# Kernel tuning notes

Measured on AMD Instinct MI355X. Metric: run time of the kernel, lower is better.

The kernel has to match this reference:

```python
import jax, jax.numpy as jnp
import numpy as np

B, T, D, H = 8, 4096, 1024, 1024


def setup_inputs() -> dict:
    key = jax.random.key(0)
    ks = jax.random.split(key, 8)
    s = 1.0 / np.sqrt(D)
    x = jax.random.normal(ks[0], (B, T, D), dtype=jnp.float32)
    Wq = jax.random.uniform(ks[1], (H, D), jnp.float32, -s, s)
    bq = jax.random.uniform(ks[2], (H,), jnp.float32, -s, s)
    Wk = jax.random.uniform(ks[3], (H, D), jnp.float32, -s, s)
    bk = jax.random.uniform(ks[4], (H,), jnp.float32, -s, s)
    Wv = jax.random.uniform(ks[5], (H, D), jnp.float32, -s, s)
    bv = jax.random.uniform(ks[6], (H,), jnp.float32, -s, s)
    wbias = jax.random.uniform(ks[7], (H,), jnp.float32, 0.0, 1.0)  # torch.rand
    return {"x": x, "Wq": Wq, "bq": bq, "Wk": Wk, "bk": bk, "Wv": Wv, "bv": bv, "wbias": wbias}


def reference(x, Wq, bq, Wk, bk, Wv, bv, wbias):
    # Q, K, V: [B, T, H]
    Q = jnp.einsum('btd,hd->bth', x, Wq) + bq
    K = jnp.einsum('btd,hd->bth', x, Wk) + bk
    V = jnp.einsum('btd,hd->bth', x, Wv) + bv
    Q_sig = jax.nn.sigmoid(Q)
    numer = jnp.exp(K + wbias)            # [B, T, H]
    denom = numer.sum(axis=0)             # [T, H] (faithful: sum over batch axis)
    weighted = (numer * V).sum(axis=0) / denom  # [T, H]
    Yt = Q_sig * weighted                 # broadcast -> [B, T, H]
    return Yt  # to_out is Identity since dim == hidden_dim
```

## Files before the change

### kernel.cpp

```cpp
#include <hip/hip_runtime.h>
#include <hip/hip_bf16.h>

#define B_ 8
#define T_ 4096
#define D_ 1024
#define H_ 1024

typedef __attribute__((ext_vector_type(8))) short short8;
typedef __attribute__((ext_vector_type(4))) float floatx4;

#define GLOAD16(gptr, lptr) \
  __builtin_amdgcn_global_load_lds((const __attribute__((address_space(1))) void*)(gptr), \
                                   (__attribute__((address_space(3))) void*)(lptr), 16, 0, 0)

__device__ __forceinline__ ushort f2b(float f) {
  unsigned x = __builtin_bit_cast(unsigned, f);
  unsigned r = (x + 0x7fffu + ((x >> 16) & 1u)) >> 16;
  return (ushort)r;
}
__device__ __forceinline__ float b2f(ushort u) {
  return __builtin_bit_cast(float, (unsigned)u << 16);
}

__global__ void cvt_kernel(const float* __restrict__ in, ushort* __restrict__ out, int n) {
  int idx = blockIdx.x * blockDim.x + threadIdx.x;
  int stride = gridDim.x * blockDim.x;
  for (long i = (long)idx * 8; i < n; i += (long)stride * 8) {
    const float4 f0 = *(const float4*)(in + i);
    const float4 f1 = *(const float4*)(in + i + 4);
    union { ushort u[8]; uint4 v; } r;
    r.u[0] = f2b(f0.x); r.u[1] = f2b(f0.y); r.u[2] = f2b(f0.z); r.u[3] = f2b(f0.w);
    r.u[4] = f2b(f1.x); r.u[5] = f2b(f1.y); r.u[6] = f2b(f1.z); r.u[7] = f2b(f1.w);
    *(uint4*)(out + i) = r.v;
  }
}

__global__ void cvt3_kernel(const float* __restrict__ w0, const float* __restrict__ w1,
                            const float* __restrict__ w2, ushort* __restrict__ out, int n) {
  const float* in = (blockIdx.y == 0) ? w0 : (blockIdx.y == 1) ? w1 : w2;
  ushort* o = out + (size_t)blockIdx.y * n;
  int idx = blockIdx.x * blockDim.x + threadIdx.x;
  int stride = gridDim.x * blockDim.x;
  for (long i = (long)idx * 8; i < n; i += (long)stride * 8) {
    const float4 f0 = *(const float4*)(in + i);
    const float4 f1 = *(const float4*)(in + i + 4);
    union { ushort u[8]; uint4 v; } r;
    r.u[0] = f2b(f0.x); r.u[1] = f2b(f0.y); r.u[2] = f2b(f0.z); r.u[3] = f2b(f0.w);
    r.u[4] = f2b(f1.x); r.u[5] = f2b(f1.y); r.u[6] = f2b(f1.z); r.u[7] = f2b(f1.w);
    *(uint4*)(o + i) = r.v;
  }
}

template <int NCOLS, bool QEPI>
__global__ __launch_bounds__(512, 2) void gemm_bt(
    const ushort* __restrict__ Am, const ushort* __restrict__ Bm,
    ushort* __restrict__ KVout, const float* __restrict__ bq,
    const float* __restrict__ weighted, float* __restrict__ out) {
  extern __shared__ ushort lds[];
  ushort* const Abuf = lds;
  ushort* const Bbuf = lds + 32768;

  const int tid = threadIdx.x;
  const int lane = tid & 63;
  const int w = tid >> 6;
  const int wr = w >> 2;
  const int wc = w & 3;
  const int R0 = blockIdx.x * 256;
  const int C0 = blockIdx.y * 256;

  const int lc = (tid & 7) ^ ((tid >> 3) & 7);
  const int r0 = ((tid >> 3) << 1) + (lc >> 2);
  const int kc0 = (lc & 3) * 8;
  const ushort* asrc = Am + (size_t)(R0 + r0) * D_ + kc0;
  const ushort* bsrc = Bm + (size_t)(C0 + r0) * D_ + kc0;

  auto stageA = [&](int t) {
    const int nb = t & 3;
    GLOAD16(asrc + t * 32, Abuf + nb * 8192 + tid * 8);
    GLOAD16(asrc + t * 32 + (size_t)128 * D_, Abuf + nb * 8192 + (512 + tid) * 8);
  };
  auto stageB = [&](int t) {
    const int nb = t & 3;
    GLOAD16(bsrc + t * 32, Bbuf + nb * 8192 + tid * 8);
    GLOAD16(bsrc + t * 32 + (size_t)128 * D_, Bbuf + nb * 8192 + (512 + tid) * 8);
  };

  const int c = lane >> 4;
  const int baseA = wr * 128 + (lane & 15);
  const int baseB = wc * 64 + (lane & 15);
  const int SA = (4 * (lane & 1) + c) ^ ((baseA >> 1) & 7);
  const int SB = (4 * (lane & 1) + c) ^ ((baseB >> 1) & 7);
  const ushort* aRd = lds + (baseA >> 1) * 64 + SA * 8;
  const ushort* bRd = lds + 32768 + (baseB >> 1) * 64 + SB * 8;

  floatx4 acc[8][4] = {};

  stageA(0); stageB(0);
  stageA(1); stageB(1);
  stageA(2); stageB(2);
  asm volatile("s_waitcnt vmcnt(8)" ::: "memory");
  __builtin_amdgcn_s_barrier();

  const int NT = D_ / 32;
  for (int t = 0; t < NT; ++t) {
    const int boff = (t & 3) * 8192;
    short8 a[4], b[4];

#pragma unroll
    for (int m = 0; m < 4; ++m) a[m] = *(const short8*)(aRd + boff + m * 512);
#pragma unroll
    for (int n = 0; n < 4; ++n) b[n] = *(const short8*)(bRd + boff + n * 512);
    if (t < NT - 3) stageA(t + 3);
    __builtin_amdgcn_s_barrier();
    asm volatile("s_waitcnt lgkmcnt(0)" ::: "memory");
    __builtin_amdgcn_sched_barrier(0);
    __builtin_amdgcn_s_setprio(1);
#pragma unroll
    for (int m = 0; m < 4; ++m)
#pragma unroll
      for (int n = 0; n < 4; ++n)
        acc[m][n] = __builtin_amdgcn_mfma_f32_16x16x32_bf16(a[m], b[n], acc[m][n], 0, 0, 0);
    __builtin_amdgcn_s_setprio(0);
    __builtin_amdgcn_s_barrier();

#pragma unroll
    for (int m = 0; m < 4; ++m) a[m] = *(const short8*)(aRd + boff + (m + 4) * 512);
    if (t < NT - 3) stageB(t + 3);
    __builtin_amdgcn_s_barrier();
    asm volatile("s_waitcnt lgkmcnt(0)" ::: "memory");
    __builtin_amdgcn_sched_barrier(0);
    __builtin_amdgcn_s_setprio(1);
#pragma unroll
    for (int m = 0; m < 4; ++m)
#pragma unroll
      for (int n = 0; n < 4; ++n)
        acc[m + 4][n] = __builtin_amdgcn_mfma_f32_16x16x32_bf16(a[m], b[n], acc[m + 4][n], 0, 0, 0);
    __builtin_amdgcn_s_setprio(0);

    if (t < NT - 3)       { asm volatile("s_waitcnt vmcnt(8)" ::: "memory"); }
    else if (t == NT - 3) { asm volatile("s_waitcnt vmcnt(4)" ::: "memory"); }
    else                  { asm volatile("s_waitcnt vmcnt(0)" ::: "memory"); }
    __builtin_amdgcn_s_barrier();
  }

  const int orow = R0 + wr * 128 + (lane >> 4) * 4;
  const int ocol = C0 + wc * 64 + (lane & 15);
  if constexpr (QEPI) {
    float bqc[4];
#pragma unroll
    for (int n = 0; n < 4; ++n) bqc[n] = bq[ocol + n * 16];
#pragma unroll
    for (int m = 0; m < 8; ++m)
#pragma unroll
      for (int n = 0; n < 4; ++n)
#pragma unroll
        for (int r = 0; r < 4; ++r) {
          int row = orow + m * 16 + r;
          int col = ocol + n * 16;
          float q = acc[m][n][r] + bqc[n];
          float sig = 1.f / (1.f + __expf(-q));
          out[(size_t)row * NCOLS + col] =
              sig * weighted[(size_t)(row & (T_ - 1)) * H_ + col];
        }
  } else {
#pragma unroll
    for (int m = 0; m < 8; ++m)
#pragma unroll
      for (int n = 0; n < 4; ++n)
#pragma unroll
        for (int r = 0; r < 4; ++r)
          KVout[(size_t)(orow + m * 16 + r) * NCOLS + ocol + n * 16] = f2b(acc[m][n][r]);
  }
}

__global__ __launch_bounds__(256) void reduce_kernel(
    const ushort* __restrict__ KV, const float* __restrict__ bk,
    const float* __restrict__ bv, const float* __restrict__ wb,
    float* __restrict__ weighted) {
  const int gid = blockIdx.x * 256 + threadIdx.x;
  const int t = gid >> 7;
  const int h0 = (gid & 127) * 8;

  float bk8[8], bv8[8], wb8[8];
#pragma unroll
  for (int j = 0; j < 8; ++j) {
    bk8[j] = bk[h0 + j];
    bv8[j] = bv[h0 + j];
    wb8[j] = wb[h0 + j];
  }

  float sn[8] = {}, sw[8] = {};
  for (int b = 0; b < B_; ++b) {
    const size_t rowoff = (size_t)(b * T_ + t) * (2 * H_);
    const short8 k8 = *(const short8*)(KV + rowoff + h0);
    const short8 v8 = *(const short8*)(KV + rowoff + H_ + h0);
#pragma unroll
    for (int j = 0; j < 8; ++j) {
      float e = __expf(b2f((ushort)k8[j]) + bk8[j] + wb8[j]);
      sn[j] += e;
      sw[j] += e * (b2f((ushort)v8[j]) + bv8[j]);
    }
  }
  float4 o0, o1;
  o0.x = sw[0] / sn[0]; o0.y = sw[1] / sn[1]; o0.z = sw[2] / sn[2]; o0.w = sw[3] / sn[3];
  o1.x = sw[4] / sn[4]; o1.y = sw[5] / sn[5]; o1.z = sw[6] / sn[6]; o1.w = sw[7] / sn[7];
  *(float4*)(weighted + (size_t)t * H_ + h0) = o0;
  *(float4*)(weighted + (size_t)t * H_ + h0 + 4) = o1;
}

extern "C" void kernel_launch(void* const* d_in, const int* in_sizes, int n_in,
                              void* d_out, int out_size, void* d_ws, size_t ws_size,
                              hipStream_t stream) {
  (void)in_sizes; (void)n_in; (void)out_size; (void)ws_size;
  const float* x = (const float*)d_in[0];
  const float* Wq = (const float*)d_in[1];
  const float* bq = (const float*)d_in[2];
  const float* Wk = (const float*)d_in[3];
  const float* bk = (const float*)d_in[4];
  const float* Wv = (const float*)d_in[5];
  const float* bv = (const float*)d_in[6];
  const float* wbias = (const float*)d_in[7];
  float* out = (float*)d_out;

  char* ws = (char*)d_ws;
  const size_t XN = (size_t)B_ * T_ * D_;
  const size_t WN = (size_t)H_ * D_;
  ushort* xb   = (ushort*)ws;
  ushort* Wqb  = (ushort*)(ws + XN * 2);
  ushort* Wkvb = Wqb + WN;
  float* weighted = (float*)(ws + XN * 2 + 3 * WN * 2);
  ushort* KV = (ushort*)(ws + XN * 2 + 3 * WN * 2 + (size_t)T_ * H_ * 4);

  (void)hipFuncSetAttribute((const void*)gemm_bt<2048, false>,
                            hipFuncAttributeMaxDynamicSharedMemorySize, 131072);
  (void)hipFuncSetAttribute((const void*)gemm_bt<1024, true>,
                            hipFuncAttributeMaxDynamicSharedMemorySize, 131072);

  cvt_kernel<<<2048, 256, 0, stream>>>(x, xb, (int)XN);
  cvt3_kernel<<<dim3(512, 3), 256, 0, stream>>>(Wq, Wk, Wv, Wqb, (int)WN);

  gemm_bt<2048, false><<<dim3((B_ * T_) / 256, 2048 / 256), 512, 131072, stream>>>(
      xb, Wkvb, KV, nullptr, nullptr, nullptr);
  reduce_kernel<<<(T_ * H_ / 8) / 256, 256, 0, stream>>>(KV, bk, bv, wbias, weighted);
  gemm_bt<1024, true><<<dim3((B_ * T_) / 256, 1024 / 256), 512, 131072, stream>>>(
      xb, Wqb, nullptr, bq, weighted, out);
}
```

Measured before the change: 328.0 us.

## Restructure GEMM mainloop to BK=64 double-buffered and stage epilogue through LDS

The bf16 GEMM mainloop changes from a 4-stage ring of K=32 tiles to a 2-stage double buffer of K=64 tiles. Each iteration is split into four MFMA phases, and global-to-LDS loads for tile t+2 are interleaved among them. The epilogue now writes accumulators into LDS first and then emits coalesced 16-byte vector stores for both the sigmoid-gated output and the bf16 KV output. This aims to cut barrier overhead per K element and replace scattered 2/4-byte global stores, at the cost of extra LDS round trips and barriers in the epilogue.

```diff
diff --git a/kernel.cpp b/kernel.cpp
--- a/kernel.cpp
+++ b/kernel.cpp
@@ -57,8 +57,6 @@
     ushort* __restrict__ KVout, const float* __restrict__ bq,
     const float* __restrict__ weighted, float* __restrict__ out) {
   extern __shared__ ushort lds[];
-  ushort* const Abuf = lds;
-  ushort* const Bbuf = lds + 32768;
 
   const int tid = threadIdx.x;
   const int lane = tid & 63;
@@ -68,49 +66,56 @@
   const int R0 = blockIdx.x * 256;
   const int C0 = blockIdx.y * 256;
 
+  const int r0 = tid >> 3;
   const int lc = (tid & 7) ^ ((tid >> 3) & 7);
-  const int r0 = ((tid >> 3) << 1) + (lc >> 2);
-  const int kc0 = (lc & 3) * 8;
-  const ushort* asrc = Am + (size_t)(R0 + r0) * D_ + kc0;
-  const ushort* bsrc = Bm + (size_t)(C0 + r0) * D_ + kc0;
-
-  auto stageA = [&](int t) {
-    const int nb = t & 3;
-    GLOAD16(asrc + t * 32, Abuf + nb * 8192 + tid * 8);
-    GLOAD16(asrc + t * 32 + (size_t)128 * D_, Abuf + nb * 8192 + (512 + tid) * 8);
+  const ushort* asrc = Am + (size_t)(R0 + r0) * D_ + lc * 8;
+  const ushort* bsrc = Bm + (size_t)(C0 + r0) * D_ + lc * 8;
+
+  auto stageA = [&](int t, int h) {
+    ushort* dst = lds + (t & 1) * 16384 + h * 8192 + tid * 8;
+    const ushort* s = asrc + t * 64 + (size_t)(h * 128) * D_;
+    GLOAD16(s, dst);
+    GLOAD16(s + (size_t)64 * D_, dst + 4096);
   };
-  auto stageB = [&](int t) {
-    const int nb = t & 3;
-    GLOAD16(bsrc + t * 32, Bbuf + nb * 8192 + tid * 8);
-    GLOAD16(bsrc + t * 32 + (size_t)128 * D_, Bbuf + nb * 8192 + (512 + tid) * 8);
+  auto stageB = [&](int t, int h) {
+    ushort* dst = lds + 32768 + (t & 1) * 16384 + h * 8192 + tid * 8;
+    const ushort* s = bsrc + t * 64 + (size_t)(h * 128) * D_;
+    GLOAD16(s, dst);
+    GLOAD16(s + (size_t)64 * D_, dst + 4096);
   };
 
-  const int c = lane >> 4;
-  const int baseA = wr * 128 + (lane & 15);
-  const int baseB = wc * 64 + (lane & 15);
-  const int SA = (4 * (lane & 1) + c) ^ ((baseA >> 1) & 7);
-  const int SB = (4 * (lane & 1) + c) ^ ((baseB >> 1) & 7);
-  const ushort* aRd = lds + (baseA >> 1) * 64 + SA * 8;
-  const ushort* bRd = lds + 32768 + (baseB >> 1) * 64 + SB * 8;
+  const int rowA = wr * 128 + (lane & 15);
+  const int rowB = wc * 64 + (lane & 15);
+  int aOff[2], bOff[2];
+#pragma unroll
+  for (int k = 0; k < 2; ++k) {
+    aOff[k] = rowA * 64 + (((k * 4) + (lane >> 4)) ^ (lane & 7)) * 8;
+    bOff[k] = rowB * 64 + (((k * 4) + (lane >> 4)) ^ (lane & 7)) * 8;
+  }
 
   floatx4 acc[8][4] = {};
-
-  stageA(0); stageB(0);
-  stageA(1); stageB(1);
-  stageA(2); stageB(2);
+  short8 aF[4][2], bA[2][2], bB[2][2];
+
+  stageB(0, 0); stageB(0, 1); stageA(0, 0); stageA(0, 1);
+  stageB(1, 0); stageB(1, 1); stageA(1, 0); stageA(1, 1);
   asm volatile("s_waitcnt vmcnt(8)" ::: "memory");
   __builtin_amdgcn_s_barrier();
 
-  const int NT = D_ / 32;
+  const int NT = D_ / 64;
   for (int t = 0; t < NT; ++t) {
-    const int boff = (t & 3) * 8192;
-    short8 a[4], b[4];
-
-#pragma unroll
-    for (int m = 0; m < 4; ++m) a[m] = *(const short8*)(aRd + boff + m * 512);
-#pragma unroll
-    for (int n = 0; n < 4; ++n) b[n] = *(const short8*)(bRd + boff + n * 512);
-    if (t < NT - 3) stageA(t + 3);
+    const ushort* Ab = lds + (t & 1) * 16384;
+    const ushort* Bb = lds + 32768 + (t & 1) * 16384;
+
+#pragma unroll
+    for (int m = 0; m < 4; ++m)
+#pragma unroll
+      for (int k = 0; k < 2; ++k)
+        aF[m][k] = *(const short8*)(Ab + m * 1024 + aOff[k]);
+#pragma unroll
+    for (int n = 0; n < 2; ++n)
+#pragma unroll
+      for (int k = 0; k < 2; ++k)
+        bA[n][k] = *(const short8*)(Bb + n * 1024 + bOff[k]);
     __builtin_amdgcn_s_barrier();
     asm volatile("s_waitcnt lgkmcnt(0)" ::: "memory");
     __builtin_amdgcn_sched_barrier(0);
@@ -118,14 +123,18 @@
 #pragma unroll
     for (int m = 0; m < 4; ++m)
 #pragma unroll
-      for (int n = 0; n < 4; ++n)
-        acc[m][n] = __builtin_amdgcn_mfma_f32_16x16x32_bf16(a[m], b[n], acc[m][n], 0, 0, 0);
+      for (int n = 0; n < 2; ++n)
+#pragma unroll
+        for (int k = 0; k < 2; ++k)
+          acc[m][n] = __builtin_amdgcn_mfma_f32_16x16x32_bf16(aF[m][k], bA[n][k], acc[m][n], 0, 0, 0);
     __builtin_amdgcn_s_setprio(0);
     __builtin_amdgcn_s_barrier();
 
 #pragma unroll
-    for (int m = 0; m < 4; ++m) a[m] = *(const short8*)(aRd + boff + (m + 4) * 512);
-    if (t < NT - 3) stageB(t + 3);
+    for (int n = 0; n < 2; ++n)
+#pragma unroll
+      for (int k = 0; k < 2; ++k)
+        bB[n][k] = *(const short8*)(Bb + (n + 2) * 1024 + bOff[k]);
     __builtin_amdgcn_s_barrier();
     asm volatile("s_waitcnt lgkmcnt(0)" ::: "memory");
     __builtin_amdgcn_sched_barrier(0);
@@ -133,43 +142,99 @@
 #pragma unroll
     for (int m = 0; m < 4; ++m)
 #pragma unroll
-      for (int n = 0; n < 4; ++n)
-        acc[m + 4][n] = __builtin_amdgcn_mfma_f32_16x16x32_bf16(a[m], b[n], acc[m + 4][n], 0, 0, 0);
+      for (int n = 0; n < 2; ++n)
+#pragma unroll
+        for (int k = 0; k < 2; ++k)
+          acc[m][n + 2] = __builtin_amdgcn_mfma_f32_16x16x32_bf16(aF[m][k], bB[n][k], acc[m][n + 2], 0, 0, 0);
     __builtin_amdgcn_s_setprio(0);
-
-    if (t < NT - 3)       { asm volatile("s_waitcnt vmcnt(8)" ::: "memory"); }
-    else if (t == NT - 3) { asm volatile("s_waitcnt vmcnt(4)" ::: "memory"); }
-    else                  { asm volatile("s_waitcnt vmcnt(0)" ::: "memory"); }
-    __builtin_amdgcn_s_barrier();
-  }
-
-  const int orow = R0 + wr * 128 + (lane >> 4) * 4;
-  const int ocol = C0 + wc * 64 + (lane & 15);
-  if constexpr (QEPI) {
-    float bqc[4];
-#pragma unroll
-    for (int n = 0; n < 4; ++n) bqc[n] = bq[ocol + n * 16];
-#pragma unroll
-    for (int m = 0; m < 8; ++m)
-#pragma unroll
-      for (int n = 0; n < 4; ++n)
-#pragma unroll
-        for (int r = 0; r < 4; ++r) {
-          int row = orow + m * 16 + r;
-          int col = ocol + n * 16;
-          float q = acc[m][n][r] + bqc[n];
-          float sig = 1.f / (1.f + __expf(-q));
-          out[(size_t)row * NCOLS + col] =
-              sig * weighted[(size_t)(row & (T_ - 1)) * H_ + col];
-        }
-  } else {
-#pragma unroll
-    for (int m = 0; m < 8; ++m)
-#pragma unroll
-      for (int n = 0; n < 4; ++n)
-#pragma unroll
-        for (int r = 0; r < 4; ++r)
-          KVout[(size_t)(orow + m * 16 + r) * NCOLS + ocol + n * 16] = f2b(acc[m][n][r]);
+    __builtin_amdgcn_s_barrier();
+
+#pragma unroll
+    for (int m = 0; m < 4; ++m)
+#pragma unroll
+      for (int k = 0; k < 2; ++k)
+        aF[m][k] = *(const short8*)(Ab + (m + 4) * 1024 + aOff[k]);
+    if (t + 2 < NT) stageB(t + 2, 0);
+    __builtin_amdgcn_s_barrier();
+    asm volatile("s_waitcnt lgkmcnt(0)" ::: "memory");
+    __builtin_amdgcn_sched_barrier(0);
+    __builtin_amdgcn_s_setprio(1);
+#pragma unroll
+    for (int m = 0; m < 4; ++m)
+#pragma unroll
+      for (int n = 0; n < 2; ++n)
+#pragma unroll
+        for (int k = 0; k < 2; ++k)
+          acc[m + 4][n] = __builtin_amdgcn_mfma_f32_16x16x32_bf16(aF[m][k], bA[n][k], acc[m + 4][n], 0, 0, 0);
+    __builtin_amdgcn_s_setprio(0);
+    __builtin_amdgcn_s_barrier();
+
+    if (t + 2 < NT) { stageB(t + 2, 1); stageA(t + 2, 0); stageA(t + 2, 1); }
+    __builtin_amdgcn_s_setprio(1);
+#pragma unroll
+    for (int m = 0; m < 4; ++m)
+#pragma unroll
+      for (int n = 0; n < 2; ++n)
+#pragma unroll
+        for (int k = 0; k < 2; ++k)
+          acc[m + 4][n + 2] = __builtin_amdgcn_mfma_f32_16x16x32_bf16(aF[m][k], bB[n][k], acc[m + 4][n + 2], 0, 0, 0);
+    __builtin_amdgcn_s_setprio(0);
+    if (t + 2 < NT) { asm volatile("s_waitcnt vmcnt(8)" ::: "memory"); }
+    else            { asm volatile("s_waitcnt vmcnt(0)" ::: "memory"); }
+    __builtin_amdgcn_s_barrier();
+  }
+
+  const int lrb = wr * 64 + (lane >> 4) * 4;
+  const int lcol = wc * 64 + (lane & 15);
+#pragma unroll
+  for (int mh = 0; mh < 2; ++mh) {
+    if (mh) __builtin_amdgcn_s_barrier();
+    if constexpr (QEPI) {
+      float* lf = (float*)lds;
+#pragma unroll
+      for (int mi = 0; mi < 4; ++mi)
+#pragma unroll
+        for (int n = 0; n < 4; ++n)
+#pragma unroll
+          for (int r = 0; r < 4; ++r)
+            lf[(lrb + mi * 16 + r) * 256 + lcol + n * 16] = acc[mh * 4 + mi][n][r];
+      __builtin_amdgcn_s_barrier();
+#pragma unroll
+      for (int j = 0; j < 16; ++j) {
+        int cidx = j * 512 + tid;
+        int lr = cidx >> 6;
+        int cc = cidx & 63;
+        int grow = R0 + (lr >> 6) * 128 + mh * 64 + (lr & 63);
+        float4 v = *(float4*)(lf + lr * 256 + cc * 4);
+        float4 bq4 = *(const float4*)(bq + C0 + cc * 4);
+        float4 wv = *(const float4*)(weighted + (size_t)(grow & (T_ - 1)) * H_ + C0 + cc * 4);
+        float4 o;
+        o.x = wv.x / (1.f + __expf(-(v.x + bq4.x)));
+        o.y = wv.y / (1.f + __expf(-(v.y + bq4.y)));
+        o.z = wv.z / (1.f + __expf(-(v.z + bq4.z)));
+        o.w = wv.w / (1.f + __expf(-(v.w + bq4.w)));
+        *(float4*)(out + (size_t)grow * NCOLS + C0 + cc * 4) = o;
+      }
+    } else {
+      ushort* lh = lds;
+#pragma unroll
+      for (int mi = 0; mi < 4; ++mi)
+#pragma unroll
+        for (int n = 0; n < 4; ++n)
+#pragma unroll
+          for (int r = 0; r < 4; ++r)
+            lh[(lrb + mi * 16 + r) * 256 + lcol + n * 16] = f2b(acc[mh * 4 + mi][n][r]);
+      __builtin_amdgcn_s_barrier();
+#pragma unroll
+      for (int j = 0; j < 8; ++j) {
+        int cidx = j * 512 + tid;
+        int lr = cidx >> 5;
+        int cc = cidx & 31;
+        int grow = R0 + (lr >> 6) * 128 + mh * 64 + (lr & 63);
+        uint4 v = *(uint4*)(lh + lr * 256 + cc * 8);
+        *(uint4*)(KVout + (size_t)grow * NCOLS + C0 + cc * 8) = v;
+      }
+    }
   }
 }
 
```

Result: faster. 314.4 us (-4.2%).

## Simplify GEMM main loop and stage epilogue through LDS for coalesced stores

Applied to the files above, without the earlier changes.

The bf16 MFMA GEMM main loop changes from a split A/B half-step schedule with a 3-deep prefetch to a single stage per K-step, prefetching 2 ahead and computing all 8x4 MFMAs per step. The LDS layout and swizzle for the operand tiles are redefined to match. The epilogue now writes accumulators to LDS in two halves and then emits vectorized float4/uint4 global stores, replacing the scattered scalar stores of the previous epilogue. This is meant to cut uncoalesced write traffic for the large Q output and the KV output. In exchange it gives up the interleaved prefetch and setprio scheduling of the old loop and adds extra barriers.

```diff
diff --git a/kernel.cpp b/kernel.cpp
--- a/kernel.cpp
+++ b/kernel.cpp
@@ -57,8 +57,6 @@
     ushort* __restrict__ KVout, const float* __restrict__ bq,
     const float* __restrict__ weighted, float* __restrict__ out) {
   extern __shared__ ushort lds[];
-  ushort* const Abuf = lds;
-  ushort* const Bbuf = lds + 32768;
 
   const int tid = threadIdx.x;
   const int lane = tid & 63;
@@ -68,108 +66,104 @@
   const int R0 = blockIdx.x * 256;
   const int C0 = blockIdx.y * 256;
 
-  const int lc = (tid & 7) ^ ((tid >> 3) & 7);
-  const int r0 = ((tid >> 3) << 1) + (lc >> 2);
-  const int kc0 = (lc & 3) * 8;
-  const ushort* asrc = Am + (size_t)(R0 + r0) * D_ + kc0;
-  const ushort* bsrc = Bm + (size_t)(C0 + r0) * D_ + kc0;
-
-  auto stageA = [&](int t) {
+  const int r0 = tid >> 2;
+  const int lc = (tid & 3) ^ ((tid >> 3) & 3);
+  const ushort* asrc = Am + (size_t)(R0 + r0) * D_ + lc * 8;
+  const ushort* bsrc = Bm + (size_t)(C0 + r0) * D_ + lc * 8;
+
+  auto stage = [&](int t) {
     const int nb = t & 3;
-    GLOAD16(asrc + t * 32, Abuf + nb * 8192 + tid * 8);
-    GLOAD16(asrc + t * 32 + (size_t)128 * D_, Abuf + nb * 8192 + (512 + tid) * 8);
+    const int kt = t * 32;
+    GLOAD16(asrc + kt, lds + nb * 8192 + tid * 8);
+    GLOAD16(asrc + kt + (size_t)128 * D_, lds + nb * 8192 + (512 + tid) * 8);
+    GLOAD16(bsrc + kt, lds + 32768 + nb * 8192 + tid * 8);
+    GLOAD16(bsrc + kt + (size_t)128 * D_, lds + 32768 + nb * 8192 + (512 + tid) * 8);
   };
-  auto stageB = [&](int t) {
-    const int nb = t & 3;
-    GLOAD16(bsrc + t * 32, Bbuf + nb * 8192 + tid * 8);
-    GLOAD16(bsrc + t * 32 + (size_t)128 * D_, Bbuf + nb * 8192 + (512 + tid) * 8);
-  };
-
-  const int c = lane >> 4;
+
   const int baseA = wr * 128 + (lane & 15);
   const int baseB = wc * 64 + (lane & 15);
-  const int SA = (4 * (lane & 1) + c) ^ ((baseA >> 1) & 7);
-  const int SB = (4 * (lane & 1) + c) ^ ((baseB >> 1) & 7);
-  const ushort* aRd = lds + (baseA >> 1) * 64 + SA * 8;
-  const ushort* bRd = lds + 32768 + (baseB >> 1) * 64 + SB * 8;
+  const int aOff = baseA * 32 + ((lane >> 4) ^ ((baseA >> 1) & 3)) * 8;
+  const int bOff = baseB * 32 + ((lane >> 4) ^ ((baseB >> 1) & 3)) * 8;
 
   floatx4 acc[8][4] = {};
 
-  stageA(0); stageB(0);
-  stageA(1); stageB(1);
-  stageA(2); stageB(2);
-  asm volatile("s_waitcnt vmcnt(8)" ::: "memory");
+  stage(0); stage(1);
+  asm volatile("s_waitcnt vmcnt(4)" ::: "memory");
   __builtin_amdgcn_s_barrier();
 
   const int NT = D_ / 32;
   for (int t = 0; t < NT; ++t) {
-    const int boff = (t & 3) * 8192;
-    short8 a[4], b[4];
-
-#pragma unroll
-    for (int m = 0; m < 4; ++m) a[m] = *(const short8*)(aRd + boff + m * 512);
-#pragma unroll
-    for (int n = 0; n < 4; ++n) b[n] = *(const short8*)(bRd + boff + n * 512);
-    if (t < NT - 3) stageA(t + 3);
-    __builtin_amdgcn_s_barrier();
-    asm volatile("s_waitcnt lgkmcnt(0)" ::: "memory");
-    __builtin_amdgcn_sched_barrier(0);
-    __builtin_amdgcn_s_setprio(1);
-#pragma unroll
-    for (int m = 0; m < 4; ++m)
+    if (t < NT - 2) stage(t + 2);
+    const ushort* Ab = lds + (t & 3) * 8192;
+    const ushort* Bb = lds + 32768 + (t & 3) * 8192;
+
+    short8 b[4], a[8];
+#pragma unroll
+    for (int n = 0; n < 4; ++n) b[n] = *(const short8*)(Bb + bOff + n * 512);
+#pragma unroll
+    for (int m = 0; m < 8; ++m) a[m] = *(const short8*)(Ab + aOff + m * 512);
+#pragma unroll
+    for (int m = 0; m < 8; ++m)
 #pragma unroll
       for (int n = 0; n < 4; ++n)
         acc[m][n] = __builtin_amdgcn_mfma_f32_16x16x32_bf16(a[m], b[n], acc[m][n], 0, 0, 0);
-    __builtin_amdgcn_s_setprio(0);
+
+    if (t < NT - 2) { asm volatile("s_waitcnt vmcnt(4)" ::: "memory"); }
+    else            { asm volatile("s_waitcnt vmcnt(0)" ::: "memory"); }
     __builtin_amdgcn_s_barrier();
-
-#pragma unroll
-    for (int m = 0; m < 4; ++m) a[m] = *(const short8*)(aRd + boff + (m + 4) * 512);
-    if (t < NT - 3) stageB(t + 3);
-    __builtin_amdgcn_s_barrier();
-    asm volatile("s_waitcnt lgkmcnt(0)" ::: "memory");
-    __builtin_amdgcn_sched_barrier(0);
-    __builtin_amdgcn_s_setprio(1);
-#pragma unroll
-    for (int m = 0; m < 4; ++m)
-#pragma unroll
-      for (int n = 0; n < 4; ++n)
-        acc[m + 4][n] = __builtin_amdgcn_mfma_f32_16x16x32_bf16(a[m], b[n], acc[m + 4][n], 0, 0, 0);
-    __builtin_amdgcn_s_setprio(0);
-
-    if (t < NT - 3)       { asm volatile("s_waitcnt vmcnt(8)" ::: "memory"); }
-    else if (t == NT - 3) { asm volatile("s_waitcnt vmcnt(4)" ::: "memory"); }
-    else                  { asm volatile("s_waitcnt vmcnt(0)" ::: "memory"); }
-    __builtin_amdgcn_s_barrier();
-  }
-
-  const int orow = R0 + wr * 128 + (lane >> 4) * 4;
-  const int ocol = C0 + wc * 64 + (lane & 15);
-  if constexpr (QEPI) {
-    float bqc[4];
-#pragma unroll
-    for (int n = 0; n < 4; ++n) bqc[n] = bq[ocol + n * 16];
-#pragma unroll
-    for (int m = 0; m < 8; ++m)
-#pragma unroll
-      for (int n = 0; n < 4; ++n)
-#pragma unroll
-        for (int r = 0; r < 4; ++r) {
-          int row = orow + m * 16 + r;
-          int col = ocol + n * 16;
-          float q = acc[m][n][r] + bqc[n];
-          float sig = 1.f / (1.f + __expf(-q));
-          out[(size_t)row * NCOLS + col] =
-              sig * weighted[(size_t)(row & (T_ - 1)) * H_ + col];
-        }
-  } else {
-#pragma unroll
-    for (int m = 0; m < 8; ++m)
-#pragma unroll
-      for (int n = 0; n < 4; ++n)
-#pragma unroll
-        for (int r = 0; r < 4; ++r)
-          KVout[(size_t)(orow + m * 16 + r) * NCOLS + ocol + n * 16] = f2b(acc[m][n][r]);
+  }
+
+  const int lrb = wr * 64 + (lane >> 4) * 4;
+  const int lcol = wc * 64 + (lane & 15);
+#pragma unroll
+  for (int mh = 0; mh < 2; ++mh) {
+    if (mh) __builtin_amdgcn_s_barrier();
+    if constexpr (QEPI) {
+      float* lf = (float*)lds;
+#pragma unroll
+      for (int mi = 0; mi < 4; ++mi)
+#pragma unroll
+        for (int n = 0; n < 4; ++n)
+#pragma unroll
+          for (int r = 0; r < 4; ++r)
+            lf[(lrb + mi * 16 + r) * 256 + lcol + n * 16] = acc[mh * 4 + mi][n][r];
+      __builtin_amdgcn_s_barrier();
+#pragma unroll
+      for (int j = 0; j < 16; ++j) {
+        int cidx = j * 512 + tid;
+        int lr = cidx >> 6;
+        int cc = cidx & 63;
+        int grow = R0 + (lr >> 6) * 128 + mh * 64 + (lr & 63);
+        float4 v = *(float4*)(lf + lr * 256 + cc * 4);
+        float4 bq4 = *(const float4*)(bq + C0 + cc * 4);
+        float4 wv = *(const float4*)(weighted + (size_t)(grow & (T_ - 1)) * H_ + C0 + cc * 4);
+        float4 o;
+        o.x = wv.x / (1.f + __expf(-(v.x + bq4.x)));
+        o.y = wv.y / (1.f + __expf(-(v.y + bq4.y)));
+        o.z = wv.z / (1.f + __expf(-(v.z + bq4.z)));
+        o.w = wv.w / (1.f + __expf(-(v.w + bq4.w)));
+        *(float4*)(out + (size_t)grow * NCOLS + C0 + cc * 4) = o;
+      }
+    } else {
+      ushort* lh = lds;
+#pragma unroll
+      for (int mi = 0; mi < 4; ++mi)
+#pragma unroll
+        for (int n = 0; n < 4; ++n)
+#pragma unroll
+          for (int r = 0; r < 4; ++r)
+            lh[(lrb + mi * 16 + r) * 256 + lcol + n * 16] = f2b(acc[mh * 4 + mi][n][r]);
+      __builtin_amdgcn_s_barrier();
+#pragma unroll
+      for (int j = 0; j < 8; ++j) {
+        int cidx = j * 512 + tid;
+        int lr = cidx >> 5;
+        int cc = cidx & 31;
+        int grow = R0 + (lr >> 6) * 128 + mh * 64 + (lr & 63);
+        uint4 v = *(uint4*)(lh + lr * 256 + cc * 8);
+        *(uint4*)(KVout + (size_t)grow * NCOLS + C0 + cc * 8) = v;
+      }
+    }
   }
 }
 
```

New measurement: 329.5 us. About the same (+0.5%).
